# Performance work log

Hardware: AMD Instinct MI355X
Metric: run time of the kernel (lower is better)

Reference implementation:

```python
import jax, jax.numpy as jnp
import numpy as np
from math import sqrt

NUM_CLASSES = 21
TOP_K = 200
CONF_THRESH = 0.01
NMS_THRESH = 0.45
VAR0, VAR1 = 0.1, 0.2
FMAPS = [19, 10, 5, 3, 2, 1]
INPUT_SIZE = 300
STEPS = [16, 32, 64, 100, 150, 300]
MIN_SIZES = [60, 105, 150, 195, 240, 285]
MAX_SIZES = [105, 150, 195, 240, 285, 330]
ASPECT_RATIOS = [[2, 3]] * 6


def _create_priorbox():
    # Faithful numpy port of create_priorbox (runs once at setup).
    mean = []
    for k, f in enumerate(FMAPS):
        f_k = INPUT_SIZE / STEPS[k]
        s_k = MIN_SIZES[k] / INPUT_SIZE
        s_kp = sqrt(s_k * (MAX_SIZES[k] / INPUT_SIZE))
        for i in range(f):
            for j in range(f):
                cx = (j + 0.5) / f_k
                cy = (i + 0.5) / f_k
                mean.append([cx, cy, s_k, s_k])
                mean.append([cx, cy, s_kp, s_kp])
                for ar in ASPECT_RATIOS[k]:
                    r = sqrt(ar)
                    mean.append([cx, cy, s_k * r, s_k / r])
                    mean.append([cx, cy, s_k / r, s_k * r])
    return np.clip(np.asarray(mean, dtype=np.float32), 0.0, 1.0)  # [3000, 4]


def setup_inputs() -> dict:
    key = jax.random.key(0)
    k1, k2 = jax.random.split(key)
    B, P, C = 8, 3000, NUM_CLASSES
    loc_data = jax.random.normal(k1, (B, P, 4), jnp.float32)
    conf_data = jax.random.uniform(k2, (B, P, C), jnp.float32)  # post-softmax-like probs
    priors = jnp.asarray(_create_priorbox())
    return {"loc_data": loc_data, "conf_data": conf_data, "priors": priors}


def _decode(loc, priors):
    # SSD box decode: center-offset form -> corner form. loc, priors: [P, 4]
    cxcy = priors[:, :2] + loc[:, :2] * VAR0 * priors[:, 2:]
    wh = priors[:, 2:] * jnp.exp(loc[:, 2:] * VAR1)
    xy1 = cxcy - 0.5 * wh
    return jnp.concatenate([xy1, xy1 + wh], axis=-1)  # [P, 4] (x1, y1, x2, y2)


def _iou_matrix(b):
    # b: [P, 4] corner-form boxes -> [P, P] pairwise IoU
    area = (b[:, 2] - b[:, 0]) * (b[:, 3] - b[:, 1])
    lt = jnp.maximum(b[:, None, :2], b[None, :, :2])
    rb = jnp.minimum(b[:, None, 2:], b[None, :, 2:])
    wh = jnp.clip(rb - lt, 0.0)
    inter = wh[..., 0] * wh[..., 1]
    union = area[:, None] + area[None, :] - inter
    return inter / jnp.maximum(union, 1e-12)


def _nms_one_class(scores, boxes):
    # scores: [P], boxes: [P, 4]. Greedy hard NMS over threshold-passing boxes,
    # kept detections (in score order) padded to TOP_K rows of [score, x1, y1, x2, y2].
    P = scores.shape[0]
    valid = scores > CONF_THRESH
    s = jnp.where(valid, scores, -jnp.inf)
    order = jnp.argsort(-s)  # descending by score; invalid sorted last
    ss = s[order]
    sb = boxes[order]
    sv = valid[order]
    iou = _iou_matrix(sb)  # [P, P]
    idx = jnp.arange(P)

    def body(i, keep):
        sup = keep[i] & (iou[i] > NMS_THRESH) & (idx > i)
        return keep & ~sup

    keep = jax.lax.stop_gradient(jax.lax.fori_loop(0, P, body, sv))
    # first TOP_K kept candidates, preserving score order
    sel = jnp.argsort(jnp.where(keep, idx, idx + P))[:TOP_K]
    ok = keep[sel]
    out_s = jnp.where(ok, ss[sel], 0.0)
    out_b = jnp.where(ok[:, None], sb[sel], 0.0)
    return jnp.concatenate([out_s[:, None], out_b], axis=-1)  # [TOP_K, 5]


def _per_image(loc, conf, priors):
    boxes = _decode(loc, priors)  # [P, 4]
    cls_scores = conf.T[1:]  # skip background class 0 -> [C-1, P]
    dets = jax.vmap(lambda s: _nms_one_class(s, boxes))(cls_scores)  # [C-1, TOP_K, 5]
    bg = jnp.zeros((1, TOP_K, 5), dets.dtype)
    return jnp.concatenate([bg, dets], axis=0)  # [C, TOP_K, 5]


def reference(loc_data, conf_data, priors):
    # lax.map over batch keeps peak memory to one image's IoU matrices.
    # NOTE: the original's final flt[(rank < top_k)].fill_(0) is a no-op in
    # PyTorch (advanced indexing returns a copy), so output is returned as-is.
    out = jax.lax.map(lambda lc: _per_image(lc[0], lc[1], priors), (loc_data, conf_data))
    return out  # [B, NUM_CLASSES, TOP_K, 5]
```

## Files before the change

kernel.cpp:

```cpp
#include <hip/hip_runtime.h>
#include <math.h>

#pragma clang fp contract(off)

#define PNUM    3000
#define NCLS    21
#define TOPK    200
#define BLOCK   1024
#define CHUNK   1024
#define NMS_T   0.45f
#define LO_BITS 0x3C23D70Bu
#define HI_BITS 0x3F800001u
#define MAXKEEP (TOPK + 64)

__device__ __constant__ unsigned LADDER[15] = {
    0x3F333333u, 0x3F266666u, 0x3F19999Au, 0x3F0CCCCDu, 0x3F000000u,
    0x3EE66666u, 0x3ECCCCCDu, 0x3EB33333u, 0x3E99999Au, 0x3E800000u,
    0x3E4CCCCDu, 0x3E19999Au, 0x3DCCCCCDu, 0x3D4CCCCDu, LO_BITS };

__device__ __forceinline__ float iou_f(float4 a, float aa, float4 b, float ab) {
    float ltx = fmaxf(a.x, b.x);
    float lty = fmaxf(a.y, b.y);
    float rbx = fminf(a.z, b.z);
    float rby = fminf(a.w, b.w);
    float iw  = fmaxf(rbx - ltx, 0.0f);
    float ih  = fmaxf(rby - lty, 0.0f);
    float inter = iw * ih;
    float uni   = aa + ab - inter;
    return inter / fmaxf(uni, 1e-12f);
}

__global__ __launch_bounds__(BLOCK) void ssd_nms_kernel(
    const float* __restrict__ loc,
    const float* __restrict__ conf,
    const float* __restrict__ priors,
    float* __restrict__ out)
{
    const int c   = blockIdx.x;
    const int b   = blockIdx.y;
    const int tid = threadIdx.x;

    float* outbase = out + ((size_t)(b * NCLS + c)) * (TOPK * 5);

    if (c == 0) {
        for (int i = tid; i < TOPK * 5; i += BLOCK) outbase[i] = 0.0f;
        return;
    }

    __shared__ unsigned long long s_bufA[CHUNK];
    __shared__ unsigned long long s_bufB[CHUNK];
    __shared__ float4             s_box[CHUNK];
    __shared__ float              s_area[CHUNK];
    __shared__ float              s_score[CHUNK];
    __shared__ float4             s_kb[MAXKEEP];
    __shared__ float              s_ka[MAXKEEP];
    __shared__ unsigned long long s_supp[64];
    __shared__ int                s_supc[64];
    __shared__ int                s_wcnt[16];
    __shared__ int s_m, s_cnt, s_done;

    const int lane = tid & 63;
    const int wav  = tid >> 6;

    unsigned hb[4];
    const float* confb = conf + ((size_t)b * PNUM) * NCLS + c;
    #pragma unroll
    for (int q = 0; q < 4; ++q) {
        int i = tid + (q << 10);
        unsigned h = 0u;
        if (i < PNUM) {
            float s = confb[(size_t)i * NCLS];
            if (s > 0.01f) h = __float_as_uint(s);
        }
        hb[q] = h;
    }
    if (tid < 64) { s_supp[lane] = 0ull; s_supc[lane] = 0; }
    if (tid == 0) { s_cnt = 0; s_done = 0; }

    unsigned Thi = HI_BITS;
    int rung = 0;
    bool done = false;

    for (;;) {
        unsigned T = LADDER[rung];

        __syncthreads();
        if (tid == 0) s_m = 0;
        s_bufA[tid] = 0ull;
        __syncthreads();
        #pragma unroll
        for (int q = 0; q < 4; ++q) {
            unsigned sb = hb[q];
            bool p = (sb >= T && sb < Thi);
            unsigned long long bal = __ballot(p);
            int wb = 0;
            if (lane == 0 && bal) wb = atomicAdd(&s_m, (int)__popcll(bal));
            wb = __shfl(wb, 0);
            if (p) {
                int dst = wb + (int)__popcll(bal & ((1ull << lane) - 1ull));
                if (dst < CHUNK) {
                    int i = tid + (q << 10);
                    s_bufA[dst] = ((unsigned long long)sb << 32) | (unsigned)(~i);
                }
            }
        }
        __syncthreads();
        int M = s_m;
        const int base0 = s_cnt;

        if (M > CHUNK) {
            unsigned lo = T + 1, hi = Thi;
            while (lo < hi) {
                unsigned mid = lo + ((hi - lo) >> 1);
                __syncthreads();
                int c2 = 0;
                #pragma unroll
                for (int q = 0; q < 4; ++q)
                    c2 += (int)__popcll(__ballot(hb[q] >= mid && hb[q] < Thi));
                if (lane == 0) s_wcnt[wav] = c2;
                __syncthreads();
                int n = 0;
                #pragma unroll
                for (int w = 0; w < 16; ++w) n += s_wcnt[w];
                if (n <= CHUNK) hi = mid; else lo = mid + 1;
            }
            T = hi;
            __syncthreads();
            int wc = 0;
            #pragma unroll
            for (int q = 0; q < 4; ++q)
                wc += (int)__popcll(__ballot(hb[q] >= T && hb[q] < Thi));
            if (lane == 0) s_wcnt[wav] = wc;
            s_bufA[tid] = 0ull;
            __syncthreads();
            int wbase = 0; M = 0;
            #pragma unroll
            for (int w = 0; w < 16; ++w) {
                int v = s_wcnt[w];
                M += v;
                if (w < wav) wbase += v;
            }
            int base = wbase;
            #pragma unroll
            for (int q = 0; q < 4; ++q) {
                unsigned sb = hb[q];
                bool p = (sb >= T && sb < Thi);
                unsigned long long bal = __ballot(p);
                if (p) {
                    int dst = base + (int)__popcll(bal & ((1ull << lane) - 1ull));
                    int i = tid + (q << 10);
                    s_bufA[dst] = ((unsigned long long)sb << 32) | (unsigned)(~i);
                }
                base += (int)__popcll(bal);
            }
            __syncthreads();
        }

        if (M == 0) {
            if (T <= LO_BITS) break;
            Thi = T;
            while (rung < 14 && LADDER[rung] >= T) rung++;
            continue;
        }

        unsigned N = 64;
        while (N < (unsigned)M) N <<= 1;
        unsigned long long key = s_bufA[tid];
        int parity = 0;
        for (unsigned k = 2; k <= N; k <<= 1) {
            for (unsigned j = k >> 1; j > 0; j >>= 1) {
                unsigned long long pk;
                if (j >= 64) {
                    unsigned long long* buf = parity ? s_bufB : s_bufA;
                    buf[tid] = key;
                    __syncthreads();
                    pk = buf[tid ^ j];
                    parity ^= 1;
                } else {
                    pk = __shfl_xor(key, (int)j, 64);
                }
                bool takeMax  = (((tid & j) == 0) == ((tid & k) == 0));
                bool pGreater = pk > key;
                if (takeMax == pGreater) key = pk;
            }
        }

        if (key != 0ull) {
            unsigned idx = ~(unsigned)key;
            float4 l  = ((const float4*)loc)[(size_t)b * PNUM + idx];
            float4 pr = ((const float4*)priors)[idx];
            float cx = pr.x + l.x * 0.1f * pr.z;
            float cy = pr.y + l.y * 0.1f * pr.w;
            float w  = pr.z * expf(l.z * 0.2f);
            float h  = pr.w * expf(l.w * 0.2f);
            float x1 = cx - 0.5f * w;
            float y1 = cy - 0.5f * h;
            float x2 = x1 + w;
            float y2 = y1 + h;
            s_box[tid]   = make_float4(x1, y1, x2, y2);
            s_area[tid]  = (x2 - x1) * (y2 - y1);
            s_score[tid] = __uint_as_float((unsigned)(key >> 32));
        }
        __syncthreads();

        int Mlive = M;
        if (base0 > 0) {
            float4 bx = make_float4(0.f, 0.f, 0.f, 0.f);
            float  ar = 0.f, sc = 0.f;
            bool alive = false;
            if (tid < M) {
                bx = s_box[tid]; ar = s_area[tid]; sc = s_score[tid];
                alive = true;
                for (int K = 0; K < base0; ++K) {
                    if (iou_f(s_kb[K], s_ka[K], bx, ar) > NMS_T) { alive = false; break; }
                }
            }
            unsigned long long bal = __ballot(alive);
            if (lane == 0) s_wcnt[wav] = (int)__popcll(bal);
            __syncthreads();
            int basew = 0, tot = 0;
            #pragma unroll
            for (int w = 0; w < 16; ++w) {
                int v = s_wcnt[w];
                tot += v;
                if (w < wav) basew += v;
            }
            if (alive) {
                int dst = basew + (int)__popcll(bal & ((1ull << lane) - 1ull));
                s_box[dst] = bx; s_area[dst] = ar; s_score[dst] = sc;
            }
            Mlive = tot;
            __syncthreads();
        }
        if (Mlive == 0) {
            if (T <= LO_BITS) break;
            Thi = T;
            while (rung < 14 && LADDER[rung] >= T) rung++;
            continue;
        }

        int pos = 0;
        while (pos < Mlive) {
            int bn  = Mlive - pos; if (bn > 64) bn = 64;
            int cnt = s_cnt;

            if (lane < bn) {
                float4 bL = s_box[pos + lane];
                float  aL = s_area[pos + lane];
                bool bad = false;
                #pragma unroll 2
                for (int K = base0 + wav; K < cnt; K += 16)
                    bad |= (iou_f(s_kb[K], s_ka[K], bL, aL) > NMS_T);
                if (bad) s_supc[lane] = 1;
                unsigned long long bits = 0ull;
                int M0 = wav << 2;
                #pragma unroll
                for (int q2 = 0; q2 < 4; ++q2) {
                    int Mi = M0 + q2;
                    if (Mi < lane) {
                        if (iou_f(s_box[pos + Mi], s_area[pos + Mi], bL, aL) > NMS_T)
                            bits |= (1ull << Mi);
                    }
                }
                if (bits) atomicOr(&s_supp[lane], bits);
            }
            __syncthreads();

            if (tid < 64) {
                unsigned long long own      = s_supp[lane];
                unsigned long long deadmask = __ballot(s_supc[lane] != 0);
                bool alive = (lane < bn) && !((deadmask >> lane) & 1ull);
                unsigned long long kept = __ballot(alive && own == 0ull);
                unsigned long long rem0 = __ballot((own & kept) != 0ull);
                unsigned long long cand = __ballot(alive && own != 0ull) & ~rem0;
                while (cand) {
                    int i = __ffsll(cand) - 1;
                    kept |= 1ull << i;
                    unsigned long long vic = __ballot(((own >> i) & 1ull) != 0ull);
                    cand &= ~vic;
                    cand &= ~(1ull << i);
                }
                int keptN = (int)__popcll(kept);
                bool me   = (kept >> lane) & 1ull;
                int krank = (int)__popcll(kept & ((1ull << lane) - 1ull));
                if (me) {
                    int kid = cnt + krank;
                    float4 bx = s_box[pos + lane];
                    s_kb[kid] = bx;
                    s_ka[kid] = s_area[pos + lane];
                    if (kid < TOPK) {
                        float* o = outbase + (size_t)kid * 5;
                        o[0] = s_score[pos + lane];
                        o[1] = bx.x; o[2] = bx.y; o[3] = bx.z; o[4] = bx.w;
                    }
                }
                s_supp[lane] = 0ull;
                s_supc[lane] = 0;
                if (lane == 0) {
                    s_cnt  = cnt + keptN;
                    s_done = (cnt + keptN >= TOPK) ? 1 : 0;
                }
            }
            __syncthreads();
            if (s_done) { done = true; break; }
            pos += bn;
        }

        if (done) break;
        if (T <= LO_BITS) break;
        Thi = T;
        while (rung < 14 && LADDER[rung] >= T) rung++;
    }

    const int cf = s_cnt < TOPK ? s_cnt : TOPK;
    for (int r = cf + tid; r < TOPK; r += BLOCK) {
        float* o = outbase + (size_t)r * 5;
        o[0] = 0.f; o[1] = 0.f; o[2] = 0.f; o[3] = 0.f; o[4] = 0.f;
    }
}

extern "C" void kernel_launch(void* const* d_in, const int* in_sizes, int n_in,
                              void* d_out, int out_size, void* d_ws, size_t ws_size,
                              hipStream_t stream) {
    const float* loc    = (const float*)d_in[0];
    const float* conf   = (const float*)d_in[1];
    const float* priors = (const float*)d_in[2];
    float* out          = (float*)d_out;
    const int B = in_sizes[0] / (PNUM * 4);
    dim3 grid(NCLS, B);
    ssd_nms_kernel<<<grid, BLOCK, 0, stream>>>(loc, conf, priors, out);
}
```

Baseline: 90.18 us.

## Predecode all boxes into shared memory and fuse bitonic LDS stages

Each block now decodes all 3000 prior boxes into shared memory once at kernel start. Candidates are then carried through sort, compaction and NMS as 64-bit keys that index this table, replacing the per-rung gather and decode from global memory. The bitonic sort also merges two LDS-exchange stages per barrier, cutting the number of __syncthreads. The cost is about 60KB of extra shared memory per block, which may lower occupancy, and every block decodes boxes redundantly, including ones that are never used.

```diff
diff --git a/kernel.cpp b/kernel.cpp
--- a/kernel.cpp
+++ b/kernel.cpp
@@ -49,9 +49,8 @@
 
     __shared__ unsigned long long s_bufA[CHUNK];
     __shared__ unsigned long long s_bufB[CHUNK];
-    __shared__ float4             s_box[CHUNK];
-    __shared__ float              s_area[CHUNK];
-    __shared__ float              s_score[CHUNK];
+    __shared__ float4             s_allbox[PNUM];
+    __shared__ float              s_allarea[PNUM];
     __shared__ float4             s_kb[MAXKEEP];
     __shared__ float              s_ka[MAXKEEP];
     __shared__ unsigned long long s_supp[64];
@@ -74,6 +73,22 @@
         }
         hb[q] = h;
     }
+
+    for (int i = tid; i < PNUM; i += BLOCK) {
+        float4 l  = ((const float4*)loc)[(size_t)b * PNUM + i];
+        float4 pr = ((const float4*)priors)[i];
+        float cx = pr.x + l.x * 0.1f * pr.z;
+        float cy = pr.y + l.y * 0.1f * pr.w;
+        float w  = pr.z * expf(l.z * 0.2f);
+        float h  = pr.w * expf(l.w * 0.2f);
+        float x1 = cx - 0.5f * w;
+        float y1 = cy - 0.5f * h;
+        float x2 = x1 + w;
+        float y2 = y1 + h;
+        s_allbox[i]  = make_float4(x1, y1, x2, y2);
+        s_allarea[i] = (x2 - x1) * (y2 - y1);
+    }
+
     if (tid < 64) { s_supp[lane] = 0ull; s_supc[lane] = 0; }
     if (tid == 0) { s_cnt = 0; s_done = 0; }
 
@@ -168,48 +183,52 @@
         unsigned long long key = s_bufA[tid];
         int parity = 0;
         for (unsigned k = 2; k <= N; k <<= 1) {
-            for (unsigned j = k >> 1; j > 0; j >>= 1) {
-                unsigned long long pk;
-                if (j >= 64) {
-                    unsigned long long* buf = parity ? s_bufB : s_bufA;
-                    buf[tid] = key;
-                    __syncthreads();
-                    pk = buf[tid ^ j];
-                    parity ^= 1;
+            unsigned j = k >> 1;
+            while (j >= 64) {
+                unsigned long long* buf = parity ? s_bufB : s_bufA;
+                unsigned j2 = j >> 1;
+                buf[tid] = key;
+                __syncthreads();
+                if (j2 >= 64) {
+                    unsigned long long a  = buf[tid ^ j];
+                    unsigned long long b2 = buf[tid ^ j2];
+                    unsigned long long c2 = buf[tid ^ (j | j2)];
+                    bool up   = ((tid & k) == 0);
+                    bool tmj  = ((tid & j)  == 0) == up;
+                    unsigned long long m1 = (tmj  == (a  > key)) ? a  : key;
+                    unsigned long long m2 = (tmj  == (c2 > b2 )) ? c2 : b2;
+                    bool tmj2 = ((tid & j2) == 0) == up;
+                    key = (tmj2 == (m2 > m1)) ? m2 : m1;
+                    j >>= 2;
                 } else {
-                    pk = __shfl_xor(key, (int)j, 64);
-                }
-                bool takeMax  = (((tid & j) == 0) == ((tid & k) == 0));
-                bool pGreater = pk > key;
-                if (takeMax == pGreater) key = pk;
-            }
-        }
-
-        if (key != 0ull) {
-            unsigned idx = ~(unsigned)key;
-            float4 l  = ((const float4*)loc)[(size_t)b * PNUM + idx];
-            float4 pr = ((const float4*)priors)[idx];
-            float cx = pr.x + l.x * 0.1f * pr.z;
-            float cy = pr.y + l.y * 0.1f * pr.w;
-            float w  = pr.z * expf(l.z * 0.2f);
-            float h  = pr.w * expf(l.w * 0.2f);
-            float x1 = cx - 0.5f * w;
-            float y1 = cy - 0.5f * h;
-            float x2 = x1 + w;
-            float y2 = y1 + h;
-            s_box[tid]   = make_float4(x1, y1, x2, y2);
-            s_area[tid]  = (x2 - x1) * (y2 - y1);
-            s_score[tid] = __uint_as_float((unsigned)(key >> 32));
-        }
-        __syncthreads();
+                    unsigned long long pk = buf[tid ^ j];
+                    bool tm = ((tid & j) == 0) == ((tid & k) == 0);
+                    if (tm == (pk > key)) key = pk;
+                    j >>= 1;
+                }
+                parity ^= 1;
+            }
+            for (; j > 0; j >>= 1) {
+                unsigned long long pk = __shfl_xor(key, (int)j, 64);
+                bool tm = ((tid & j) == 0) == ((tid & k) == 0);
+                if (tm == (pk > key)) key = pk;
+            }
+        }
+
+        __syncthreads();
+        s_bufA[tid] = key;
+        __syncthreads();
+        unsigned long long* keys = s_bufA;
 
         int Mlive = M;
         if (base0 > 0) {
-            float4 bx = make_float4(0.f, 0.f, 0.f, 0.f);
-            float  ar = 0.f, sc = 0.f;
+            unsigned long long kk = 0ull;
             bool alive = false;
             if (tid < M) {
-                bx = s_box[tid]; ar = s_area[tid]; sc = s_score[tid];
+                kk = keys[tid];
+                unsigned idx = ~(unsigned)kk;
+                float4 bx = s_allbox[idx];
+                float  ar = s_allarea[idx];
                 alive = true;
                 for (int K = 0; K < base0; ++K) {
                     if (iou_f(s_kb[K], s_ka[K], bx, ar) > NMS_T) { alive = false; break; }
@@ -225,11 +244,10 @@
                 tot += v;
                 if (w < wav) basew += v;
             }
-            if (alive) {
-                int dst = basew + (int)__popcll(bal & ((1ull << lane) - 1ull));
-                s_box[dst] = bx; s_area[dst] = ar; s_score[dst] = sc;
-            }
+            if (alive)
+                s_bufB[basew + (int)__popcll(bal & ((1ull << lane) - 1ull))] = kk;
             Mlive = tot;
+            keys = s_bufB;
             __syncthreads();
         }
         if (Mlive == 0) {
@@ -245,8 +263,9 @@
             int cnt = s_cnt;
 
             if (lane < bn) {
-                float4 bL = s_box[pos + lane];
-                float  aL = s_area[pos + lane];
+                unsigned idxL = ~(unsigned)keys[pos + lane];
+                float4 bL = s_allbox[idxL];
+                float  aL = s_allarea[idxL];
                 bool bad = false;
                 #pragma unroll 2
                 for (int K = base0 + wav; K < cnt; K += 16)
@@ -258,7 +277,8 @@
                 for (int q2 = 0; q2 < 4; ++q2) {
                     int Mi = M0 + q2;
                     if (Mi < lane) {
-                        if (iou_f(s_box[pos + Mi], s_area[pos + Mi], bL, aL) > NMS_T)
+                        unsigned idxJ = ~(unsigned)keys[pos + Mi];
+                        if (iou_f(s_allbox[idxJ], s_allarea[idxJ], bL, aL) > NMS_T)
                             bits |= (1ull << Mi);
                     }
                 }
@@ -285,12 +305,14 @@
                 int krank = (int)__popcll(kept & ((1ull << lane) - 1ull));
                 if (me) {
                     int kid = cnt + krank;
-                    float4 bx = s_box[pos + lane];
+                    unsigned long long kk = keys[pos + lane];
+                    unsigned idx = ~(unsigned)kk;
+                    float4 bx = s_allbox[idx];
                     s_kb[kid] = bx;
-                    s_ka[kid] = s_area[pos + lane];
+                    s_ka[kid] = s_allarea[idx];
                     if (kid < TOPK) {
                         float* o = outbase + (size_t)kid * 5;
-                        o[0] = s_score[pos + lane];
+                        o[0] = __uint_as_float((unsigned)(kk >> 32));
                         o[1] = bx.x; o[2] = bx.y; o[3] = bx.z; o[4] = bx.w;
                     }
                 }
```

Result: no change. 90.03 us (-0.2%).
